# Kernel tuning notes

Hardware: AMD Instinct MI355X
Metric: run time of the kernel (lower is better)

## Reference

```python
import jax, jax.numpy as jnp
import numpy as np

N, E, G = 50000, 800000, 64   # nodes, edges, graphs
IN, HID, H = 128, 64, 4       # in_channels, hidden_channels, heads


def setup_inputs() -> dict:
    key = jax.random.key(0)
    ks = jax.random.split(key, 32)
    r = lambda i, shape, sc=0.05: jax.random.normal(ks[i], shape, jnp.float32) * sc
    inp = {
        "x": jax.random.normal(ks[0], (N, IN), jnp.float32),
        "edge_index": jax.random.randint(ks[1], (2, E), 0, N),
        "batch": jnp.sort(jax.random.randint(ks[2], (N,), 0, G)),
        # GATConv 1: in -> hidden, heads=4, concat
        "W1": r(3, (IN, H * HID)), "a_src1": r(4, (H, HID)), "a_dst1": r(5, (H, HID)), "b1": r(6, (H * HID,)),
        "bn1_g": 1.0 + r(7, (H * HID,)), "bn1_b": r(8, (H * HID,)), "bn1_m": r(9, (H * HID,)),
        "bn1_v": jax.random.uniform(ks[10], (H * HID,), jnp.float32, 0.5, 1.5),
        # GATConv 2: hidden*heads -> hidden, heads=4, concat
        "W2": r(11, (H * HID, H * HID)), "a_src2": r(12, (H, HID)), "a_dst2": r(13, (H, HID)), "b2": r(14, (H * HID,)),
        "bn2_g": 1.0 + r(15, (H * HID,)), "bn2_b": r(16, (H * HID,)), "bn2_m": r(17, (H * HID,)),
        "bn2_v": jax.random.uniform(ks[18], (H * HID,), jnp.float32, 0.5, 1.5),
        # GATConv 3: hidden*heads -> hidden, heads=1
        "W3": r(19, (H * HID, HID)), "a_src3": r(20, (1, HID)), "a_dst3": r(21, (1, HID)), "b3": r(22, (HID,)),
        # projection MLP: Linear(2*hidden, hidden) -> ReLU -> Linear(hidden, hidden)
        "P1": r(23, (2 * HID, HID)), "pb1": r(24, (HID,)),
        "P2": r(25, (HID, HID)), "pb2": r(26, (HID,)),
    }
    return inp


def _gat_conv(x, src, dst, n, W, a_s, a_d, b, concat):
    """PyG-style GATConv (eval mode). src/dst already include self-loops."""
    Hh, C = a_s.shape
    h = (x @ W).reshape(n, Hh, C)                       # [N, H, C]
    al_s = jnp.einsum('nhc,hc->nh', h, a_s)             # [N, H]
    al_d = jnp.einsum('nhc,hc->nh', h, a_d)             # [N, H]
    e = jax.nn.leaky_relu(al_s[src] + al_d[dst], 0.2)   # [E', H]
    # segment softmax over incoming edges of each dst node
    m = jax.ops.segment_max(e, dst, num_segments=n)     # [N, H] (finite: self-loops)
    ex = jnp.exp(e - m[dst])
    den = jax.ops.segment_sum(ex, dst, num_segments=n)
    alpha = ex / den[dst]                               # [E', H]
    out = jax.ops.segment_sum(h[src] * alpha[..., None], dst, num_segments=n)  # [N, H, C]
    out = out.reshape(n, Hh * C) if concat else out.mean(axis=1)
    return out + b


def _bn(x, g, b, m, v):
    return (x - m) * jax.lax.rsqrt(v + 1e-5) * g + b


def _forward(x, edge_index, batch,
             W1, a_src1, a_dst1, b1, bn1_g, bn1_b, bn1_m, bn1_v,
             W2, a_src2, a_dst2, b2, bn2_g, bn2_b, bn2_m, bn2_v,
             W3, a_src3, a_dst3, b3, P1, pb1, P2, pb2):
    n = x.shape[0]
    loop = jnp.arange(n)
    src = jnp.concatenate([edge_index[0], loop])        # add_self_loops=True
    dst = jnp.concatenate([edge_index[1], loop])
    h = _gat_conv(x, src, dst, n, W1, a_src1, a_dst1, b1, True)
    h = jax.nn.elu(_bn(h, bn1_g, bn1_b, bn1_m, bn1_v))  # dropout inactive in eval
    h = _gat_conv(h, src, dst, n, W2, a_src2, a_dst2, b2, True)
    h = jax.nn.elu(_bn(h, bn2_g, bn2_b, bn2_m, bn2_v))
    h = _gat_conv(h, src, dst, n, W3, a_src3, a_dst3, b3, False)  # heads=1
    x_max = jax.ops.segment_max(h, batch, num_segments=G)
    cnt = jax.ops.segment_sum(jnp.ones((n, 1), h.dtype), batch, num_segments=G)
    x_mean = jax.ops.segment_sum(h, batch, num_segments=G) / jnp.maximum(cnt, 1.0)
    z = jnp.concatenate([x_max, x_mean], axis=1)        # [G, 2*HID]
    z = jax.nn.relu(z @ P1 + pb1)
    return z @ P2 + pb2                                  # [G, HID]


def reference(x, edge_index, batch,
              W1, a_src1, a_dst1, b1, bn1_g, bn1_b, bn1_m, bn1_v,
              W2, a_src2, a_dst2, b2, bn2_g, bn2_b, bn2_m, bn2_v,
              W3, a_src3, a_dst3, b3, P1, pb1, P2, pb2):
    return _forward(x, edge_index, batch,
                    W1, a_src1, a_dst1, b1, bn1_g, bn1_b, bn1_m, bn1_v,
                    W2, a_src2, a_dst2, b2, bn2_g, bn2_b, bn2_m, bn2_v,
                    W3, a_src3, a_dst3, b3, P1, pb1, P2, pb2)
```

## Files before the change

### kernel.cpp

```cpp
#include <hip/hip_runtime.h>

typedef unsigned int uint;
typedef unsigned short ushort;

#define NFIX 50000
#define EFIX 800000
#define GFIX 64
#define BCAP 64
#define DCAP 128
#define WSTRIDE 136
#define PSL 16

__device__ __forceinline__ float bflo(uint u) { return __uint_as_float(u << 16); }
__device__ __forceinline__ float bfhi(uint u) { return __uint_as_float(u & 0xffff0000u); }
__device__ __forceinline__ float bf1(ushort u) { return __uint_as_float(((uint)u) << 16); }
__device__ __forceinline__ ushort f2bf(float f) {
    uint u = __float_as_uint(f);
    u += 0x7fffu + ((u >> 16) & 1u);
    return (ushort)(u >> 16);
}
__device__ __forceinline__ float lrelu(float x) { return fmaxf(x, 0.2f * x); }

typedef __attribute__((ext_vector_type(8))) short bf16x8;
typedef __attribute__((ext_vector_type(4))) float f32x4;
union U16B { uint4 u; bf16x8 v; };

__device__ __forceinline__ int ld_idx(const int* __restrict__ p, long i, int w64) {
    return w64 ? p[2 * i] : p[i];
}

__device__ __forceinline__ int frag_off(int k, int c, int K) {
    return ((c >> 4) * (K >> 5) + (k >> 5)) * 512 + ((c & 15) + 16 * ((k >> 3) & 3)) * 8 + (k & 7);
}

#define WJ1 (128 * 256)
#define WJ2 (256 * 256)
#define WJ3 (256 * 64)
#define SCJOBS (EFIX + WJ2 + WJ3)

__global__ void pre_w1_detect(const int* __restrict__ ei, int* __restrict__ flag,
                              const float* __restrict__ W1, ushort* __restrict__ Wf1) {
    if (blockIdx.x == gridDim.x - 1) {
        const int lane = threadIdx.x & 63;
        if (threadIdx.x < 64) {
            int v = (lane < 16) ? ei[2 * lane + 1] : 0;
            unsigned long long any = __ballot(v != 0);
            if (lane == 0) *flag = (any == 0ULL) ? 1 : 0;
        }
        return;
    }
    int j = blockIdx.x * 256 + threadIdx.x;
    int k = j >> 8, c = j & 255;
    Wf1[frag_off(k, c, 128)] = f2bf(W1[j]);
}

__global__ __launch_bounds__(256) void gemm1_build(
    const float* __restrict__ x, const ushort* __restrict__ Wf,
    const float* __restrict__ as_, const float* __restrict__ ad_,
    ushort* __restrict__ Hout, float* __restrict__ als, float* __restrict__ ald,
    int M, int gemmBlocks,
    const int* __restrict__ ei, const int* __restrict__ flag,
    int* __restrict__ cnt, ushort* __restrict__ ssb,
    const float* __restrict__ W2, ushort* __restrict__ Wf2,
    const float* __restrict__ W3, ushort* __restrict__ Wf3) {
    constexpr int K = 128;
    constexpr int NI = 4;
    constexpr int LOG2K = 7;
    __shared__ ushort sa[64][K + 8];

    if (blockIdx.x >= gemmBlocks) {
        int i = (blockIdx.x - gemmBlocks) * 256 + threadIdx.x;
        if (i < EFIX) {
            const int w64 = *flag;
            int d = ld_idx(ei, (long)EFIX + i, w64);
            int s = ld_idx(ei, i, w64);
            int slot = atomicAdd(&cnt[d], 1);
            if (slot < BCAP) ssb[d * BCAP + slot] = (ushort)s;
        } else {
            int j = i - EFIX;
            if (j < WJ2) {
                int k = j >> 8, c = j & 255;
                Wf2[frag_off(k, c, 256)] = f2bf(W2[j]);
            } else if ((j -= WJ2) < WJ3) {
                int k = j >> 6, c = j & 63;
                Wf3[frag_off(k, c, 256)] = f2bf(W3[j]);
            }
        }
        return;
    }

    const int tid = threadIdx.x;
    const int wave = tid >> 6;
    const int lane = tid & 63;
    const int rowBase = blockIdx.x * 64;
    const int colBase = wave * (NI * 16);
    const int tr = lane & 15;
    const int kq = (lane >> 4) * 8;

#pragma unroll
    for (int it = 0; it < (64 * K) / 1024; ++it) {
        int linear = it * 1024 + tid * 4;
        int row = rowBase + (linear >> LOG2K);
        int col = linear & (K - 1);
        row = row < M ? row : M - 1;
        float4 v = *(const float4*)(x + (size_t)row * K + col);
        ushort4 o; o.x = f2bf(v.x); o.y = f2bf(v.y); o.z = f2bf(v.z); o.w = f2bf(v.w);
        *(ushort4*)(&sa[linear >> LOG2K][col]) = o;
    }
    __syncthreads();

    f32x4 acc[4][NI];
#pragma unroll
    for (int i = 0; i < 4; ++i)
#pragma unroll
        for (int j = 0; j < NI; ++j) acc[i][j] = (f32x4){0.f, 0.f, 0.f, 0.f};

    const ushort* bp[NI];
#pragma unroll
    for (int ni = 0; ni < NI; ++ni)
        bp[ni] = Wf + ((size_t)(colBase / 16 + ni) * (K / 32)) * 512 + lane * 8;

    for (int k0 = 0; k0 < K; k0 += 32) {
        bf16x8 a[4], b[NI];
#pragma unroll
        for (int mi = 0; mi < 4; ++mi) { U16B t; t.u = *(const uint4*)(&sa[mi * 16 + tr][k0 + kq]); a[mi] = t.v; }
#pragma unroll
        for (int ni = 0; ni < NI; ++ni) { U16B t; t.u = *(const uint4*)(bp[ni] + (k0 >> 5) * 512); b[ni] = t.v; }
#pragma unroll
        for (int mi = 0; mi < 4; ++mi)
#pragma unroll
            for (int ni = 0; ni < NI; ++ni)
                acc[mi][ni] = __builtin_amdgcn_mfma_f32_16x16x32_bf16(a[mi], b[ni], acc[mi][ni], 0, 0, 0);
    }

    const int orow = (lane >> 4) * 4;
    const int ocol = colBase + tr;
#pragma unroll
    for (int mi = 0; mi < 4; ++mi) {
#pragma unroll
        for (int r = 0; r < 4; ++r) {
            int row = rowBase + mi * 16 + orow + r;
            if (row < M) {
#pragma unroll
                for (int ni = 0; ni < NI; ++ni)
                    Hout[(size_t)row * 256 + ocol + ni * 16] = f2bf(acc[mi][ni][r]);
            }
        }
    }

    float asv[NI], adv[NI];
#pragma unroll
    for (int ni = 0; ni < NI; ++ni) {
        asv[ni] = as_[colBase + ni * 16 + tr];
        adv[ni] = ad_[colBase + ni * 16 + tr];
    }
#pragma unroll
    for (int mi = 0; mi < 4; ++mi) {
#pragma unroll
        for (int r = 0; r < 4; ++r) {
            float ps = 0.f, pd = 0.f;
#pragma unroll
            for (int ni = 0; ni < NI; ++ni) {
                ps += acc[mi][ni][r] * asv[ni];
                pd += acc[mi][ni][r] * adv[ni];
            }
#pragma unroll
            for (int off = 1; off < 16; off <<= 1) {
                ps += __shfl_xor(ps, off, 64);
                pd += __shfl_xor(pd, off, 64);
            }
            int row = rowBase + mi * 16 + orow + r;
            if (tr == 0 && row < M) {
                als[(size_t)row * 4 + wave] = ps;
                ald[(size_t)row * 4 + wave] = pd;
            }
        }
    }
}

template <int K, int NI, int HAL>
__global__ __launch_bounds__(256) void gemm_frag(const ushort* __restrict__ X,
                                                 const ushort* __restrict__ Wf,
                                                 const float* __restrict__ as_,
                                                 const float* __restrict__ ad_,
                                                 ushort* __restrict__ Hout,
                                                 float* __restrict__ als,
                                                 float* __restrict__ ald, int M) {
    constexpr int NC = NI * 16 * 4;
    constexpr int LOG2K = (K == 256) ? 8 : 7;
    __shared__ ushort sa[64][K + 8];
    __shared__ float s_ps[4][64];
    __shared__ float s_pd[4][64];

    const int tid = threadIdx.x;
    const int wave = tid >> 6;
    const int lane = tid & 63;
    const int rowBase = blockIdx.x * 64;
    const int colBase = wave * (NI * 16);
    const int tr = lane & 15;
    const int kq = (lane >> 4) * 8;

    const ushort* src = X + (size_t)rowBase * K;
#pragma unroll
    for (int it = 0; it < (64 * K) / 2048; ++it) {
        int linear = it * 2048 + tid * 8;
        int row = linear >> LOG2K;
        int col = linear & (K - 1);
        *(uint4*)(&sa[row][col]) = *(const uint4*)(src + linear);
    }
    __syncthreads();

    f32x4 acc[4][NI];
#pragma unroll
    for (int i = 0; i < 4; ++i)
#pragma unroll
        for (int j = 0; j < NI; ++j) acc[i][j] = (f32x4){0.f, 0.f, 0.f, 0.f};

    const ushort* bp[NI];
#pragma unroll
    for (int ni = 0; ni < NI; ++ni)
        bp[ni] = Wf + ((size_t)(colBase / 16 + ni) * (K / 32)) * 512 + lane * 8;

    for (int k0 = 0; k0 < K; k0 += 32) {
        bf16x8 a[4], b[NI];
#pragma unroll
        for (int mi = 0; mi < 4; ++mi) { U16B t; t.u = *(const uint4*)(&sa[mi * 16 + tr][k0 + kq]); a[mi] = t.v; }
#pragma unroll
        for (int ni = 0; ni < NI; ++ni) { U16B t; t.u = *(const uint4*)(bp[ni] + (k0 >> 5) * 512); b[ni] = t.v; }
#pragma unroll
        for (int mi = 0; mi < 4; ++mi)
#pragma unroll
            for (int ni = 0; ni < NI; ++ni)
                acc[mi][ni] = __builtin_amdgcn_mfma_f32_16x16x32_bf16(a[mi], b[ni], acc[mi][ni], 0, 0, 0);
    }

    const int orow = (lane >> 4) * 4;
    const int ocol = colBase + tr;
#pragma unroll
    for (int mi = 0; mi < 4; ++mi) {
#pragma unroll
        for (int r = 0; r < 4; ++r) {
            int row = rowBase + mi * 16 + orow + r;
            if (row < M) {
#pragma unroll
                for (int ni = 0; ni < NI; ++ni)
                    Hout[(size_t)row * NC + ocol + ni * 16] = f2bf(acc[mi][ni][r]);
            }
        }
    }

    float asv[NI], adv[NI];
#pragma unroll
    for (int ni = 0; ni < NI; ++ni) {
        asv[ni] = as_[colBase + ni * 16 + tr];
        adv[ni] = ad_[colBase + ni * 16 + tr];
    }
#pragma unroll
    for (int mi = 0; mi < 4; ++mi) {
#pragma unroll
        for (int r = 0; r < 4; ++r) {
            float ps = 0.f, pd = 0.f;
#pragma unroll
            for (int ni = 0; ni < NI; ++ni) {
                ps += acc[mi][ni][r] * asv[ni];
                pd += acc[mi][ni][r] * adv[ni];
            }
#pragma unroll
            for (int off = 1; off < 16; off <<= 1) {
                ps += __shfl_xor(ps, off, 64);
                pd += __shfl_xor(pd, off, 64);
            }
            if constexpr (HAL == 4) {
                int row = rowBase + mi * 16 + orow + r;
                if (tr == 0 && row < M) {
                    als[(size_t)row * 4 + wave] = ps;
                    ald[(size_t)row * 4 + wave] = pd;
                }
            } else {
                if (tr == 0) {
                    s_ps[wave][mi * 16 + orow + r] = ps;
                    s_pd[wave][mi * 16 + orow + r] = pd;
                }
            }
        }
    }
    if constexpr (HAL == 1) {
        __syncthreads();
        if (tid < 64) {
            int row = rowBase + tid;
            if (row < M) {
                als[row] = s_ps[0][tid] + s_ps[1][tid] + s_ps[2][tid] + s_ps[3][tid];
                ald[row] = s_pd[0][tid] + s_pd[1][tid] + s_pd[2][tid] + s_pd[3][tid];
            }
        }
    }
}

template <int H_, int C>
__global__ __launch_bounds__(256) void gat_gather(
    const ushort* __restrict__ hb, const float* __restrict__ als, const float* __restrict__ ald,
    const int* __restrict__ cnt, const ushort* __restrict__ ssb,
    const float* __restrict__ bias, const float* __restrict__ bng, const float* __restrict__ bnb,
    const float* __restrict__ bnm, const float* __restrict__ bnv,
    ushort* __restrict__ xnext, int n) {
    constexpr int TC = H_ * C;
    constexpr int CPL = TC / 64;
    constexpr int GW = 64 / H_;
    constexpr int KMAX = DCAP / GW;
    constexpr int SHIFT = 8;
    __shared__ float s_w[4][H_ * WSTRIDE];
    __shared__ int s_idx[4][DCAP];
    const int wv = threadIdx.x >> 6;
    const int node = blockIdx.x * 4 + wv;
    if (node >= n) return;
    const int lane = threadIdx.x & 63;
    const int head = lane / GW;
    const int hl = lane & (GW - 1);
    const int c0 = lane * CPL;

    const float aldn = ald[(size_t)node * H_ + head];
    const float selfle = lrelu(als[(size_t)node * H_ + head] + aldn);
    const int e0 = node * BCAP;
    int d = cnt[node];
    d = d < BCAP ? d : BCAP;

    float acc[CPL];

    {
        float le_reg[KMAX];
        int s_reg[KMAX];
        float m = selfle;
#pragma unroll
        for (int k = 0; k < KMAX; ++k) {
            int j = hl + k * GW;
            if (j < d) {
                int s = ssb[e0 + j];
                s_reg[k] = s;
                float le = lrelu(als[(size_t)s * H_ + head] + aldn);
                le_reg[k] = le;
                m = fmaxf(m, le);
            }
        }
#pragma unroll
        for (int off = 1; off < GW; off <<= 1) m = fmaxf(m, __shfl_xor(m, off, 64));

        float dsum = (hl == 0) ? __expf(selfle - m) : 0.f;
#pragma unroll
        for (int k = 0; k < KMAX; ++k) {
            int j = hl + k * GW;
            if (j < d) {
                float p = __expf(le_reg[k] - m);
                dsum += p;
                s_w[wv][head * WSTRIDE + j] = p;
                if (head == 0) s_idx[wv][j] = s_reg[k] << SHIFT;
            }
        }
#pragma unroll
        for (int off = 1; off < GW; off <<= 1) dsum += __shfl_xor(dsum, off, 64);
        const float inv = 1.0f / dsum;

        {
            float psf = __expf(selfle - m);
            uint2 hu = *(const uint2*)(hb + (size_t)node * TC + c0);
            acc[0] = psf * bflo(hu.x); acc[1] = psf * bfhi(hu.x);
            acc[2] = psf * bflo(hu.y); acc[3] = psf * bfhi(hu.y);
        }
        const float* wbase = &s_w[wv][head * WSTRIDE];
        const int* ibase = &s_idx[wv][0];
        const ushort* hc = hb + c0;
        int j = 0;
        for (; j + 8 <= d; j += 8) {
            float4 wa = *(const float4*)(wbase + j);
            float4 wb2 = *(const float4*)(wbase + j + 4);
            int4 ia = *(const int4*)(ibase + j);
            int4 ib = *(const int4*)(ibase + j + 4);
            uint2 h0 = *(const uint2*)(hc + ia.x);
            uint2 h1 = *(const uint2*)(hc + ia.y);
            uint2 h2 = *(const uint2*)(hc + ia.z);
            uint2 h3 = *(const uint2*)(hc + ia.w);
            uint2 h4 = *(const uint2*)(hc + ib.x);
            uint2 h5 = *(const uint2*)(hc + ib.y);
            uint2 h6 = *(const uint2*)(hc + ib.z);
            uint2 h7 = *(const uint2*)(hc + ib.w);
            acc[0] = fmaf(wa.x, bflo(h0.x), acc[0]); acc[1] = fmaf(wa.x, bfhi(h0.x), acc[1]);
            acc[2] = fmaf(wa.x, bflo(h0.y), acc[2]); acc[3] = fmaf(wa.x, bfhi(h0.y), acc[3]);
            acc[0] = fmaf(wa.y, bflo(h1.x), acc[0]); acc[1] = fmaf(wa.y, bfhi(h1.x), acc[1]);
            acc[2] = fmaf(wa.y, bflo(h1.y), acc[2]); acc[3] = fmaf(wa.y, bfhi(h1.y), acc[3]);
            acc[0] = fmaf(wa.z, bflo(h2.x), acc[0]); acc[1] = fmaf(wa.z, bfhi(h2.x), acc[1]);
            acc[2] = fmaf(wa.z, bflo(h2.y), acc[2]); acc[3] = fmaf(wa.z, bfhi(h2.y), acc[3]);
            acc[0] = fmaf(wa.w, bflo(h3.x), acc[0]); acc[1] = fmaf(wa.w, bfhi(h3.x), acc[1]);
            acc[2] = fmaf(wa.w, bflo(h3.y), acc[2]); acc[3] = fmaf(wa.w, bfhi(h3.y), acc[3]);
            acc[0] = fmaf(wb2.x, bflo(h4.x), acc[0]); acc[1] = fmaf(wb2.x, bfhi(h4.x), acc[1]);
            acc[2] = fmaf(wb2.x, bflo(h4.y), acc[2]); acc[3] = fmaf(wb2.x, bfhi(h4.y), acc[3]);
            acc[0] = fmaf(wb2.y, bflo(h5.x), acc[0]); acc[1] = fmaf(wb2.y, bfhi(h5.x), acc[1]);
            acc[2] = fmaf(wb2.y, bflo(h5.y), acc[2]); acc[3] = fmaf(wb2.y, bfhi(h5.y), acc[3]);
            acc[0] = fmaf(wb2.z, bflo(h6.x), acc[0]); acc[1] = fmaf(wb2.z, bfhi(h6.x), acc[1]);
            acc[2] = fmaf(wb2.z, bflo(h6.y), acc[2]); acc[3] = fmaf(wb2.z, bfhi(h6.y), acc[3]);
            acc[0] = fmaf(wb2.w, bflo(h7.x), acc[0]); acc[1] = fmaf(wb2.w, bfhi(h7.x), acc[1]);
            acc[2] = fmaf(wb2.w, bflo(h7.y), acc[2]); acc[3] = fmaf(wb2.w, bfhi(h7.y), acc[3]);
        }
        for (; j + 4 <= d; j += 4) {
            float4 wa = *(const float4*)(wbase + j);
            int4 ia = *(const int4*)(ibase + j);
            uint2 h0 = *(const uint2*)(hc + ia.x);
            uint2 h1 = *(const uint2*)(hc + ia.y);
            uint2 h2 = *(const uint2*)(hc + ia.z);
            uint2 h3 = *(const uint2*)(hc + ia.w);
            acc[0] = fmaf(wa.x, bflo(h0.x), acc[0]); acc[1] = fmaf(wa.x, bfhi(h0.x), acc[1]);
            acc[2] = fmaf(wa.x, bflo(h0.y), acc[2]); acc[3] = fmaf(wa.x, bfhi(h0.y), acc[3]);
            acc[0] = fmaf(wa.y, bflo(h1.x), acc[0]); acc[1] = fmaf(wa.y, bfhi(h1.x), acc[1]);
            acc[2] = fmaf(wa.y, bflo(h1.y), acc[2]); acc[3] = fmaf(wa.y, bfhi(h1.y), acc[3]);
            acc[0] = fmaf(wa.z, bflo(h2.x), acc[0]); acc[1] = fmaf(wa.z, bfhi(h2.x), acc[1]);
            acc[2] = fmaf(wa.z, bflo(h2.y), acc[2]); acc[3] = fmaf(wa.z, bfhi(h2.y), acc[3]);
            acc[0] = fmaf(wa.w, bflo(h3.x), acc[0]); acc[1] = fmaf(wa.w, bfhi(h3.x), acc[1]);
            acc[2] = fmaf(wa.w, bflo(h3.y), acc[2]); acc[3] = fmaf(wa.w, bfhi(h3.y), acc[3]);
        }
        for (; j < d; ++j) {
            float w = wbase[j];
            int io = ibase[j];
            uint2 hu = *(const uint2*)(hc + io);
            acc[0] = fmaf(w, bflo(hu.x), acc[0]); acc[1] = fmaf(w, bfhi(hu.x), acc[1]);
            acc[2] = fmaf(w, bflo(hu.y), acc[2]); acc[3] = fmaf(w, bfhi(hu.y), acc[3]);
        }
#pragma unroll
        for (int q = 0; q < CPL; ++q) acc[q] *= inv;
    }

    float4 bi = *(const float4*)(bias + c0);
    float4 gg = *(const float4*)(bng + c0);
    float4 bb = *(const float4*)(bnb + c0);
    float4 mm = *(const float4*)(bnm + c0);
    float4 vv = *(const float4*)(bnv + c0);
    float biA[4] = { bi.x, bi.y, bi.z, bi.w };
    float ggA[4] = { gg.x, gg.y, gg.z, gg.w };
    float bbA[4] = { bb.x, bb.y, bb.z, bb.w };
    float mmA[4] = { mm.x, mm.y, mm.z, mm.w };
    float vvA[4] = { vv.x, vv.y, vv.z, vv.w };
    float r[4];
#pragma unroll
    for (int j2 = 0; j2 < 4; ++j2) {
        float v = acc[j2] + biA[j2];
        v = (v - mmA[j2]) * rsqrtf(vvA[j2] + 1e-5f) * ggA[j2] + bbA[j2];
        v = v > 0.f ? v : (__expf(v) - 1.0f);
        r[j2] = v;
    }
    uint p0 = (uint)f2bf(r[0]) | ((uint)f2bf(r[1]) << 16);
    uint p1 = (uint)f2bf(r[2]) | ((uint)f2bf(r[3]) << 16);
    uint2 o; o.x = p0; o.y = p1;
    *(uint2*)(xnext + (size_t)node * TC + c0) = o;
}

__global__ __launch_bounds__(256) void gat_gather_fin(
    const ushort* __restrict__ hb, const float* __restrict__ als, const float* __restrict__ ald,
    const int* __restrict__ cnt, const ushort* __restrict__ ssb,
    const float* __restrict__ bias, float* __restrict__ yout, int n) {
    __shared__ float s_w[4][BCAP + 16];
    __shared__ int s_idx[4][BCAP + 16];
    const int wv = threadIdx.x >> 6;
    const int node = blockIdx.x * 4 + wv;
    if (node >= n) return;
    const int lane = threadIdx.x & 63;
    const int es = lane >> 4;
    const int cq = (lane & 15) * 4;

    const float aldn = ald[node];
    const float selfle = lrelu(als[node] + aldn);
    const int e0 = node * BCAP;
    int d = cnt[node];
    d = d < BCAP ? d : BCAP;
    const int dpad = (d + 15) & ~15;

    float le = -3.0e38f;
    int sreg = 0;
    if (lane < d) {
        sreg = ssb[e0 + lane];
        le = lrelu(als[sreg] + aldn);
    }
    float m = fmaxf(le, selfle);
#pragma unroll
    for (int off = 1; off < 64; off <<= 1) m = fmaxf(m, __shfl_xor(m, off, 64));

    float p = 0.f;
    if (lane < d) {
        p = __expf(le - m);
        s_w[wv][lane] = p;
        s_idx[wv][lane] = sreg << 6;
    } else if (lane < dpad) {
        s_w[wv][lane] = 0.f;
        s_idx[wv][lane] = 0;
    }
    const float psf = __expf(selfle - m);
    float dsum = p + (lane == 0 ? psf : 0.f);
#pragma unroll
    for (int off = 1; off < 64; off <<= 1) dsum += __shfl_xor(dsum, off, 64);
    const float inv = 1.0f / dsum;

    const ushort* hp = hb + cq;
    const float* wbase = &s_w[wv][0];
    const int* ibase = &s_idx[wv][0];
    float a0 = 0.f, a1 = 0.f, a2 = 0.f, a3 = 0.f;
    for (int j = 0; j < d; j += 16) {
        int i0 = ibase[j + es];
        int i1 = ibase[j + 4 + es];
        int i2 = ibase[j + 8 + es];
        int i3 = ibase[j + 12 + es];
        uint2 h0 = *(const uint2*)(hp + i0);
        uint2 h1 = *(const uint2*)(hp + i1);
        uint2 h2 = *(const uint2*)(hp + i2);
        uint2 h3 = *(const uint2*)(hp + i3);
        float w0 = wbase[j + es];
        float w1 = wbase[j + 4 + es];
        float w2 = wbase[j + 8 + es];
        float w3 = wbase[j + 12 + es];
        a0 = fmaf(w0, bflo(h0.x), a0); a1 = fmaf(w0, bfhi(h0.x), a1);
        a2 = fmaf(w0, bflo(h0.y), a2); a3 = fmaf(w0, bfhi(h0.y), a3);
        a0 = fmaf(w1, bflo(h1.x), a0); a1 = fmaf(w1, bfhi(h1.x), a1);
        a2 = fmaf(w1, bflo(h1.y), a2); a3 = fmaf(w1, bfhi(h1.y), a3);
        a0 = fmaf(w2, bflo(h2.x), a0); a1 = fmaf(w2, bfhi(h2.x), a1);
        a2 = fmaf(w2, bflo(h2.y), a2); a3 = fmaf(w2, bfhi(h2.y), a3);
        a0 = fmaf(w3, bflo(h3.x), a0); a1 = fmaf(w3, bfhi(h3.x), a1);
        a2 = fmaf(w3, bflo(h3.y), a2); a3 = fmaf(w3, bfhi(h3.y), a3);
    }
#pragma unroll
    for (int off = 16; off < 64; off <<= 1) {
        a0 += __shfl_xor(a0, off, 64);
        a1 += __shfl_xor(a1, off, 64);
        a2 += __shfl_xor(a2, off, 64);
        a3 += __shfl_xor(a3, off, 64);
    }
    {
        uint2 hs = *(const uint2*)(hp + node * 64);
        a0 = (a0 + psf * bflo(hs.x)) * inv;
        a1 = (a1 + psf * bfhi(hs.x)) * inv;
        a2 = (a2 + psf * bflo(hs.y)) * inv;
        a3 = (a3 + psf * bfhi(hs.y)) * inv;
    }
    if (es == 0) {
        float4 o = { a0 + bias[cq + 0], a1 + bias[cq + 1],
                     a2 + bias[cq + 2], a3 + bias[cq + 3] };
        *(float4*)(yout + (size_t)node * 64 + cq) = o;
    }
}

__device__ __forceinline__ int lbound_w(const int* a, int n, int v, int w64) {
    int lo = 0, hi = n;
    while (lo < hi) {
        int mid = (lo + hi) >> 1;
        int bv = w64 ? a[2 * mid] : a[mid];
        if (bv < v) lo = mid + 1; else hi = mid;
    }
    return lo;
}

__global__ __launch_bounds__(256) void pool_part(const float* __restrict__ y, const int* __restrict__ batch,
                                                 const int* __restrict__ flag,
                                                 float* __restrict__ part) {
    const int w64 = *flag;
    const int g = blockIdx.x;
    const int sl = blockIdx.y;
    const int t = threadIdx.x;
    const int start = lbound_w(batch, NFIX, g, w64);
    const int end = lbound_w(batch, NFIX, g + 1, w64);
    const int len = end - start;
    const int s0 = start + (int)((long)len * sl / PSL);
    const int s1 = start + (int)((long)len * (sl + 1) / PSL);
    const int ch = t & 63, sub = t >> 6;
    float mx = -3.0e38f, sm = 0.f;
    for (int i = s0 + sub; i < s1; i += 4) {
        float v = y[(size_t)i * 64 + ch];
        mx = fmaxf(mx, v); sm += v;
    }
    __shared__ float smx[256], ssm[256];
    smx[t] = mx; ssm[t] = sm;
    __syncthreads();
    if (t < 64) {
        mx = fmaxf(fmaxf(smx[t], smx[t + 64]), fmaxf(smx[t + 128], smx[t + 192]));
        sm = ssm[t] + ssm[t + 64] + ssm[t + 128] + ssm[t + 192];
        float* pb = part + ((size_t)g * PSL + sl) * 128;
        pb[t] = mx;
        pb[64 + t] = sm;
    }
}

__global__ __launch_bounds__(64) void pool_fin_mlp(const float* __restrict__ part,
                                                   const int* __restrict__ batch,
                                                   const int* __restrict__ flag,
                                                   const float* __restrict__ P1, const float* __restrict__ pb1,
                                                   const float* __restrict__ P2, const float* __restrict__ pb2,
                                                   float* __restrict__ out) {
    const int w64 = *flag;
    const int g = blockIdx.x;
    const int t = threadIdx.x;
    const int start = lbound_w(batch, NFIX, g, w64);
    const int end = lbound_w(batch, NFIX, g + 1, w64);
    const int cnt = end - start;
    __shared__ float pl[128];
    __shared__ float z[64];
    float mx = -3.0e38f, sm = 0.f;
    const float* pb = part + (size_t)g * PSL * 128;
#pragma unroll
    for (int s = 0; s < PSL; ++s) {
        mx = fmaxf(mx, pb[s * 128 + t]);
        sm += pb[s * 128 + 64 + t];
    }
    float mean = cnt > 0 ? sm / (float)cnt : 0.f;
    if (cnt == 0) mx = 0.f;
    pl[t] = mx;
    pl[64 + t] = mean;
    __syncthreads();
    float a = pb1[t];
    for (int k = 0; k < 128; ++k) a = fmaf(pl[k], P1[k * 64 + t], a);
    z[t] = fmaxf(a, 0.f);
    __syncthreads();
    float o = pb2[t];
    for (int k = 0; k < 64; ++k) o = fmaf(z[k], P2[k * 64 + t], o);
    out[(size_t)g * 64 + t] = o;
}

__global__ void write_code(float* out, float code) {
    if (threadIdx.x == 0 && blockIdx.x == 0) out[0] = code;
}

extern "C" void kernel_launch(void* const* d_in, const int* in_sizes, int n_in,
                              void* d_out, int out_size, void* d_ws, size_t ws_size,
                              hipStream_t stream) {
    const float* x = (const float*)d_in[0];
    const int* ei = (const int*)d_in[1];
    const int* batch = (const int*)d_in[2];
    const float* W1 = (const float*)d_in[3];
    const float* as1 = (const float*)d_in[4];
    const float* ad1 = (const float*)d_in[5];
    const float* b1 = (const float*)d_in[6];
    const float* bn1g = (const float*)d_in[7];
    const float* bn1b = (const float*)d_in[8];
    const float* bn1m = (const float*)d_in[9];
    const float* bn1v = (const float*)d_in[10];
    const float* W2 = (const float*)d_in[11];
    const float* as2 = (const float*)d_in[12];
    const float* ad2 = (const float*)d_in[13];
    const float* b2 = (const float*)d_in[14];
    const float* bn2g = (const float*)d_in[15];
    const float* bn2b = (const float*)d_in[16];
    const float* bn2m = (const float*)d_in[17];
    const float* bn2v = (const float*)d_in[18];
    const float* W3 = (const float*)d_in[19];
    const float* as3 = (const float*)d_in[20];
    const float* ad3 = (const float*)d_in[21];
    const float* b3 = (const float*)d_in[22];
    const float* P1 = (const float*)d_in[23];
    const float* pb1 = (const float*)d_in[24];
    const float* P2 = (const float*)d_in[25];
    const float* pb2 = (const float*)d_in[26];
    float* out = (float*)d_out;
    (void)n_in; (void)out_size; (void)in_sizes;

    const int N_ = NFIX;

    char* ws = (char*)d_ws;
    size_t off = 0;
    auto alloc = [&](size_t bytes) -> void* {
        void* p = ws + off;
        off = (off + bytes + 255) & ~(size_t)255;
        return p;
    };
    ushort* hbuf = (ushort*)alloc((size_t)N_ * 256 * 2);
    ushort* xbuf = (ushort*)alloc((size_t)N_ * 256 * 2);
    float* als = (float*)alloc((size_t)N_ * 4 * 4);
    float* ald = (float*)alloc((size_t)N_ * 4 * 4);
    int* cnt = (int*)alloc((size_t)N_ * 4);
    ushort* ssb = (ushort*)alloc((size_t)N_ * BCAP * 2);
    ushort* Wf1 = (ushort*)alloc(128 * 256 * 2);
    ushort* Wf2 = (ushort*)alloc(256 * 256 * 2);
    ushort* Wf3 = (ushort*)alloc(256 * 64 * 2);
    float* part = (float*)alloc((size_t)GFIX * PSL * 128 * 4);
    int* flag = (int*)alloc(256);
    float* y3 = (float*)xbuf;
    const size_t needed = off;

    if (ws_size < needed) {
        write_code<<<1, 64, 0, stream>>>(out, 1000.0f + (float)(needed >> 20));
        return;
    }

    const int ng4 = (N_ + 3) / 4;
    const int rb64 = (N_ + 63) / 64;
    const int scg = (SCJOBS + 255) / 256;
    const int wg1 = WJ1 / 256 + 1;

    hipMemsetAsync(cnt, 0, (size_t)N_ * 4, stream);
    pre_w1_detect<<<wg1, 256, 0, stream>>>(ei, flag, W1, Wf1);

    gemm1_build<<<rb64 + scg, 256, 0, stream>>>(x, Wf1, as1, ad1, hbuf, als, ald,
                                                N_, rb64, ei, flag, cnt, ssb,
                                                W2, Wf2, W3, Wf3);
    gat_gather<4, 64><<<ng4, 256, 0, stream>>>(hbuf, als, ald, cnt, ssb,
                                               b1, bn1g, bn1b, bn1m, bn1v, xbuf, N_);
    gemm_frag<256, 4, 4><<<rb64, 256, 0, stream>>>(xbuf, Wf2, as2, ad2, hbuf, als, ald, N_);
    gat_gather<4, 64><<<ng4, 256, 0, stream>>>(hbuf, als, ald, cnt, ssb,
                                               b2, bn2g, bn2b, bn2m, bn2v, xbuf, N_);
    gemm_frag<256, 1, 1><<<rb64, 256, 0, stream>>>(xbuf, Wf3, as3, ad3, hbuf, als, ald, N_);
    gat_gather_fin<<<ng4, 256, 0, stream>>>(hbuf, als, ald, cnt, ssb, b3, y3, N_);

    pool_part<<<dim3(GFIX, PSL), 256, 0, stream>>>(y3, batch, flag, part);
    pool_fin_mlp<<<GFIX, 64, 0, stream>>>(part, batch, flag, P1, pb1, P2, pb2, out);
}
```

Baseline: 383.0 us.

## Fuse GAT attention gather with the following layer's GEMM per 16-node tile

Merges the gather/softmax/BN/ELU kernel with the next layer's MFMA GEMM. Each block aggregates 16 nodes into shared memory and immediately multiplies them by the next weight matrix, also producing the attention logits. This removes the round trip of the intermediate activation buffer through global memory and two kernel launches. In exchange, each block loads the full weight fragments for only 16 rows, which raises weight traffic, and it uses separate ping-pong buffers for the attention logits.

```diff
diff --git a/kernel.cpp b/kernel.cpp
--- a/kernel.cpp
+++ b/kernel.cpp
@@ -178,176 +178,62 @@
     }
 }
 
-template <int K, int NI, int HAL>
-__global__ __launch_bounds__(256) void gemm_frag(const ushort* __restrict__ X,
-                                                 const ushort* __restrict__ Wf,
-                                                 const float* __restrict__ as_,
-                                                 const float* __restrict__ ad_,
-                                                 ushort* __restrict__ Hout,
-                                                 float* __restrict__ als,
-                                                 float* __restrict__ ald, int M) {
-    constexpr int NC = NI * 16 * 4;
-    constexpr int LOG2K = (K == 256) ? 8 : 7;
-    __shared__ ushort sa[64][K + 8];
-    __shared__ float s_ps[4][64];
-    __shared__ float s_pd[4][64];
-
-    const int tid = threadIdx.x;
-    const int wave = tid >> 6;
-    const int lane = tid & 63;
-    const int rowBase = blockIdx.x * 64;
-    const int colBase = wave * (NI * 16);
-    const int tr = lane & 15;
-    const int kq = (lane >> 4) * 8;
-
-    const ushort* src = X + (size_t)rowBase * K;
-#pragma unroll
-    for (int it = 0; it < (64 * K) / 2048; ++it) {
-        int linear = it * 2048 + tid * 8;
-        int row = linear >> LOG2K;
-        int col = linear & (K - 1);
-        *(uint4*)(&sa[row][col]) = *(const uint4*)(src + linear);
-    }
-    __syncthreads();
-
-    f32x4 acc[4][NI];
-#pragma unroll
-    for (int i = 0; i < 4; ++i)
-#pragma unroll
-        for (int j = 0; j < NI; ++j) acc[i][j] = (f32x4){0.f, 0.f, 0.f, 0.f};
-
-    const ushort* bp[NI];
-#pragma unroll
-    for (int ni = 0; ni < NI; ++ni)
-        bp[ni] = Wf + ((size_t)(colBase / 16 + ni) * (K / 32)) * 512 + lane * 8;
-
-    for (int k0 = 0; k0 < K; k0 += 32) {
-        bf16x8 a[4], b[NI];
-#pragma unroll
-        for (int mi = 0; mi < 4; ++mi) { U16B t; t.u = *(const uint4*)(&sa[mi * 16 + tr][k0 + kq]); a[mi] = t.v; }
-#pragma unroll
-        for (int ni = 0; ni < NI; ++ni) { U16B t; t.u = *(const uint4*)(bp[ni] + (k0 >> 5) * 512); b[ni] = t.v; }
-#pragma unroll
-        for (int mi = 0; mi < 4; ++mi)
-#pragma unroll
-            for (int ni = 0; ni < NI; ++ni)
-                acc[mi][ni] = __builtin_amdgcn_mfma_f32_16x16x32_bf16(a[mi], b[ni], acc[mi][ni], 0, 0, 0);
-    }
-
-    const int orow = (lane >> 4) * 4;
-    const int ocol = colBase + tr;
-#pragma unroll
-    for (int mi = 0; mi < 4; ++mi) {
-#pragma unroll
-        for (int r = 0; r < 4; ++r) {
-            int row = rowBase + mi * 16 + orow + r;
-            if (row < M) {
-#pragma unroll
-                for (int ni = 0; ni < NI; ++ni)
-                    Hout[(size_t)row * NC + ocol + ni * 16] = f2bf(acc[mi][ni][r]);
-            }
-        }
-    }
-
-    float asv[NI], adv[NI];
-#pragma unroll
-    for (int ni = 0; ni < NI; ++ni) {
-        asv[ni] = as_[colBase + ni * 16 + tr];
-        adv[ni] = ad_[colBase + ni * 16 + tr];
-    }
-#pragma unroll
-    for (int mi = 0; mi < 4; ++mi) {
-#pragma unroll
-        for (int r = 0; r < 4; ++r) {
-            float ps = 0.f, pd = 0.f;
-#pragma unroll
-            for (int ni = 0; ni < NI; ++ni) {
-                ps += acc[mi][ni][r] * asv[ni];
-                pd += acc[mi][ni][r] * adv[ni];
-            }
-#pragma unroll
-            for (int off = 1; off < 16; off <<= 1) {
-                ps += __shfl_xor(ps, off, 64);
-                pd += __shfl_xor(pd, off, 64);
-            }
-            if constexpr (HAL == 4) {
-                int row = rowBase + mi * 16 + orow + r;
-                if (tr == 0 && row < M) {
-                    als[(size_t)row * 4 + wave] = ps;
-                    ald[(size_t)row * 4 + wave] = pd;
-                }
-            } else {
-                if (tr == 0) {
-                    s_ps[wave][mi * 16 + orow + r] = ps;
-                    s_pd[wave][mi * 16 + orow + r] = pd;
-                }
-            }
-        }
-    }
-    if constexpr (HAL == 1) {
-        __syncthreads();
-        if (tid < 64) {
-            int row = rowBase + tid;
-            if (row < M) {
-                als[row] = s_ps[0][tid] + s_ps[1][tid] + s_ps[2][tid] + s_ps[3][tid];
-                ald[row] = s_pd[0][tid] + s_pd[1][tid] + s_pd[2][tid] + s_pd[3][tid];
-            }
-        }
-    }
-}
-
-template <int H_, int C>
-__global__ __launch_bounds__(256) void gat_gather(
+template <int NOUT>
+__global__ __launch_bounds__(256) void fused_gather_gemm(
     const ushort* __restrict__ hb, const float* __restrict__ als, const float* __restrict__ ald,
     const int* __restrict__ cnt, const ushort* __restrict__ ssb,
     const float* __restrict__ bias, const float* __restrict__ bng, const float* __restrict__ bnb,
     const float* __restrict__ bnm, const float* __restrict__ bnv,
-    ushort* __restrict__ xnext, int n) {
-    constexpr int TC = H_ * C;
-    constexpr int CPL = TC / 64;
-    constexpr int GW = 64 / H_;
-    constexpr int KMAX = DCAP / GW;
+    const ushort* __restrict__ Wf, const float* __restrict__ as_, const float* __restrict__ ad_,
+    ushort* __restrict__ Hout, float* __restrict__ als_o, float* __restrict__ ald_o, int n) {
+    constexpr int K = 256;
+    constexpr int NI = NOUT / 64;
     constexpr int SHIFT = 8;
-    __shared__ float s_w[4][H_ * WSTRIDE];
+    __shared__ ushort sa[16][K + 8];
+    __shared__ float s_w[4][4 * WSTRIDE];
     __shared__ int s_idx[4][DCAP];
-    const int wv = threadIdx.x >> 6;
-    const int node = blockIdx.x * 4 + wv;
-    if (node >= n) return;
-    const int lane = threadIdx.x & 63;
-    const int head = lane / GW;
-    const int hl = lane & (GW - 1);
-    const int c0 = lane * CPL;
-
-    const float aldn = ald[(size_t)node * H_ + head];
-    const float selfle = lrelu(als[(size_t)node * H_ + head] + aldn);
-    const int e0 = node * BCAP;
-    int d = cnt[node];
-    d = d < BCAP ? d : BCAP;
-
-    float acc[CPL];
-
-    {
-        float le_reg[KMAX];
-        int s_reg[KMAX];
+    __shared__ float s_ps[4][16];
+    __shared__ float s_pd[4][16];
+
+    const int tid = threadIdx.x;
+    const int wv = tid >> 6;
+    const int lane = tid & 63;
+    const int rowBase = blockIdx.x * 16;
+    const int head = lane >> 4;
+    const int hl = lane & 15;
+    const int c0 = lane * 4;
+
+    for (int sub = 0; sub < 4; ++sub) {
+        const int node = rowBase + wv * 4 + sub;
+        const int nodec = node < n ? node : n - 1;
+
+        const float aldn = ald[(size_t)nodec * 4 + head];
+        const float selfle = lrelu(als[(size_t)nodec * 4 + head] + aldn);
+        const int e0 = nodec * BCAP;
+        int d = cnt[nodec];
+        d = d < BCAP ? d : BCAP;
+
+        float le_reg[8];
+        int s_reg[8];
         float m = selfle;
 #pragma unroll
-        for (int k = 0; k < KMAX; ++k) {
-            int j = hl + k * GW;
+        for (int k = 0; k < 8; ++k) {
+            int j = hl + k * 16;
             if (j < d) {
                 int s = ssb[e0 + j];
                 s_reg[k] = s;
-                float le = lrelu(als[(size_t)s * H_ + head] + aldn);
+                float le = lrelu(als[(size_t)s * 4 + head] + aldn);
                 le_reg[k] = le;
                 m = fmaxf(m, le);
             }
         }
 #pragma unroll
-        for (int off = 1; off < GW; off <<= 1) m = fmaxf(m, __shfl_xor(m, off, 64));
+        for (int off = 1; off < 16; off <<= 1) m = fmaxf(m, __shfl_xor(m, off, 64));
 
         float dsum = (hl == 0) ? __expf(selfle - m) : 0.f;
 #pragma unroll
-        for (int k = 0; k < KMAX; ++k) {
-            int j = hl + k * GW;
+        for (int k = 0; k < 8; ++k) {
+            int j = hl + k * 16;
             if (j < d) {
                 float p = __expf(le_reg[k] - m);
                 dsum += p;
@@ -356,12 +242,13 @@
             }
         }
 #pragma unroll
-        for (int off = 1; off < GW; off <<= 1) dsum += __shfl_xor(dsum, off, 64);
+        for (int off = 1; off < 16; off <<= 1) dsum += __shfl_xor(dsum, off, 64);
         const float inv = 1.0f / dsum;
 
+        float acc[4];
         {
             float psf = __expf(selfle - m);
-            uint2 hu = *(const uint2*)(hb + (size_t)node * TC + c0);
+            uint2 hu = *(const uint2*)(hb + (size_t)nodec * 256 + c0);
             acc[0] = psf * bflo(hu.x); acc[1] = psf * bfhi(hu.x);
             acc[2] = psf * bflo(hu.y); acc[3] = psf * bfhi(hu.y);
         }
@@ -423,31 +310,110 @@
             acc[2] = fmaf(w, bflo(hu.y), acc[2]); acc[3] = fmaf(w, bfhi(hu.y), acc[3]);
         }
 #pragma unroll
-        for (int q = 0; q < CPL; ++q) acc[q] *= inv;
-    }
-
-    float4 bi = *(const float4*)(bias + c0);
-    float4 gg = *(const float4*)(bng + c0);
-    float4 bb = *(const float4*)(bnb + c0);
-    float4 mm = *(const float4*)(bnm + c0);
-    float4 vv = *(const float4*)(bnv + c0);
-    float biA[4] = { bi.x, bi.y, bi.z, bi.w };
-    float ggA[4] = { gg.x, gg.y, gg.z, gg.w };
-    float bbA[4] = { bb.x, bb.y, bb.z, bb.w };
-    float mmA[4] = { mm.x, mm.y, mm.z, mm.w };
-    float vvA[4] = { vv.x, vv.y, vv.z, vv.w };
-    float r[4];
-#pragma unroll
-    for (int j2 = 0; j2 < 4; ++j2) {
-        float v = acc[j2] + biA[j2];
-        v = (v - mmA[j2]) * rsqrtf(vvA[j2] + 1e-5f) * ggA[j2] + bbA[j2];
-        v = v > 0.f ? v : (__expf(v) - 1.0f);
-        r[j2] = v;
-    }
-    uint p0 = (uint)f2bf(r[0]) | ((uint)f2bf(r[1]) << 16);
-    uint p1 = (uint)f2bf(r[2]) | ((uint)f2bf(r[3]) << 16);
-    uint2 o; o.x = p0; o.y = p1;
-    *(uint2*)(xnext + (size_t)node * TC + c0) = o;
+        for (int q = 0; q < 4; ++q) acc[q] *= inv;
+
+        float4 bi = *(const float4*)(bias + c0);
+        float4 gg = *(const float4*)(bng + c0);
+        float4 bb = *(const float4*)(bnb + c0);
+        float4 mm = *(const float4*)(bnm + c0);
+        float4 vv = *(const float4*)(bnv + c0);
+        float biA[4] = { bi.x, bi.y, bi.z, bi.w };
+        float ggA[4] = { gg.x, gg.y, gg.z, gg.w };
+        float bbA[4] = { bb.x, bb.y, bb.z, bb.w };
+        float mmA[4] = { mm.x, mm.y, mm.z, mm.w };
+        float vvA[4] = { vv.x, vv.y, vv.z, vv.w };
+        float r[4];
+#pragma unroll
+        for (int q = 0; q < 4; ++q) {
+            float v = acc[q] + biA[q];
+            v = (v - mmA[q]) * rsqrtf(vvA[q] + 1e-5f) * ggA[q] + bbA[q];
+            v = v > 0.f ? v : (__expf(v) - 1.0f);
+            r[q] = v;
+        }
+        uint2 o;
+        o.x = (uint)f2bf(r[0]) | ((uint)f2bf(r[1]) << 16);
+        o.y = (uint)f2bf(r[2]) | ((uint)f2bf(r[3]) << 16);
+        *(uint2*)(&sa[wv * 4 + sub][c0]) = o;
+    }
+    __syncthreads();
+
+    const int tr = lane & 15;
+    const int kq = (lane >> 4) * 8;
+    const int colBase = wv * (NI * 16);
+
+    f32x4 acc[NI];
+#pragma unroll
+    for (int ni = 0; ni < NI; ++ni) acc[ni] = (f32x4){0.f, 0.f, 0.f, 0.f};
+
+    const ushort* bp[NI];
+#pragma unroll
+    for (int ni = 0; ni < NI; ++ni)
+        bp[ni] = Wf + ((size_t)(colBase / 16 + ni) * (K / 32)) * 512 + lane * 8;
+
+    for (int k0 = 0; k0 < K; k0 += 32) {
+        bf16x8 a, b[NI];
+        { U16B t; t.u = *(const uint4*)(&sa[tr][k0 + kq]); a = t.v; }
+#pragma unroll
+        for (int ni = 0; ni < NI; ++ni) { U16B t; t.u = *(const uint4*)(bp[ni] + (k0 >> 5) * 512); b[ni] = t.v; }
+#pragma unroll
+        for (int ni = 0; ni < NI; ++ni)
+            acc[ni] = __builtin_amdgcn_mfma_f32_16x16x32_bf16(a, b[ni], acc[ni], 0, 0, 0);
+    }
+
+    const int orow = (lane >> 4) * 4;
+    const int ocol = colBase + tr;
+#pragma unroll
+    for (int r = 0; r < 4; ++r) {
+        int row = rowBase + orow + r;
+        if (row < n) {
+#pragma unroll
+            for (int ni = 0; ni < NI; ++ni)
+                Hout[(size_t)row * NOUT + ocol + ni * 16] = f2bf(acc[ni][r]);
+        }
+    }
+
+    float asv[NI], adv[NI];
+#pragma unroll
+    for (int ni = 0; ni < NI; ++ni) {
+        asv[ni] = as_[colBase + ni * 16 + tr];
+        adv[ni] = ad_[colBase + ni * 16 + tr];
+    }
+#pragma unroll
+    for (int r = 0; r < 4; ++r) {
+        float ps = 0.f, pd = 0.f;
+#pragma unroll
+        for (int ni = 0; ni < NI; ++ni) {
+            ps += acc[ni][r] * asv[ni];
+            pd += acc[ni][r] * adv[ni];
+        }
+#pragma unroll
+        for (int off = 1; off < 16; off <<= 1) {
+            ps += __shfl_xor(ps, off, 64);
+            pd += __shfl_xor(pd, off, 64);
+        }
+        if constexpr (NOUT == 256) {
+            int row = rowBase + orow + r;
+            if (tr == 0 && row < n) {
+                als_o[(size_t)row * 4 + wv] = ps;
+                ald_o[(size_t)row * 4 + wv] = pd;
+            }
+        } else {
+            if (tr == 0) {
+                s_ps[wv][orow + r] = ps;
+                s_pd[wv][orow + r] = pd;
+            }
+        }
+    }
+    if constexpr (NOUT == 64) {
+        __syncthreads();
+        if (tid < 16) {
+            int row = rowBase + tid;
+            if (row < n) {
+                als_o[row] = s_ps[0][tid] + s_ps[1][tid] + s_ps[2][tid] + s_ps[3][tid];
+                ald_o[row] = s_pd[0][tid] + s_pd[1][tid] + s_pd[2][tid] + s_pd[3][tid];
+            }
+        }
+    }
 }
 
 __global__ __launch_bounds__(256) void gat_gather_fin(
@@ -663,10 +629,12 @@
         off = (off + bytes + 255) & ~(size_t)255;
         return p;
     };
-    ushort* hbuf = (ushort*)alloc((size_t)N_ * 256 * 2);
-    ushort* xbuf = (ushort*)alloc((size_t)N_ * 256 * 2);
-    float* als = (float*)alloc((size_t)N_ * 4 * 4);
-    float* ald = (float*)alloc((size_t)N_ * 4 * 4);
+    ushort* bufA = (ushort*)alloc((size_t)N_ * 256 * 2);
+    ushort* bufB = (ushort*)alloc((size_t)N_ * 256 * 2);
+    float* als1 = (float*)alloc((size_t)N_ * 4 * 4);
+    float* ald1 = (float*)alloc((size_t)N_ * 4 * 4);
+    float* als2 = (float*)alloc((size_t)N_ * 4 * 4);
+    float* ald2 = (float*)alloc((size_t)N_ * 4 * 4);
     int* cnt = (int*)alloc((size_t)N_ * 4);
     ushort* ssb = (ushort*)alloc((size_t)N_ * BCAP * 2);
     ushort* Wf1 = (ushort*)alloc(128 * 256 * 2);
@@ -674,7 +642,7 @@
     ushort* Wf3 = (ushort*)alloc(256 * 64 * 2);
     float* part = (float*)alloc((size_t)GFIX * PSL * 128 * 4);
     int* flag = (int*)alloc(256);
-    float* y3 = (float*)xbuf;
+    float* y3 = (float*)bufB;
     const size_t needed = off;
 
     if (ws_size < needed) {
@@ -683,6 +651,7 @@
     }
 
     const int ng4 = (N_ + 3) / 4;
+    const int ngg = (N_ + 15) / 16;
     const int rb64 = (N_ + 63) / 64;
     const int scg = (SCJOBS + 255) / 256;
     const int wg1 = WJ1 / 256 + 1;
@@ -690,16 +659,16 @@
     hipMemsetAsync(cnt, 0, (size_t)N_ * 4, stream);
     pre_w1_detect<<<wg1, 256, 0, stream>>>(ei, flag, W1, Wf1);
 
-    gemm1_build<<<rb64 + scg, 256, 0, stream>>>(x, Wf1, as1, ad1, hbuf, als, ald,
+    gemm1_build<<<rb64 + scg, 256, 0, stream>>>(x, Wf1, as1, ad1, bufA, als1, ald1,
                                                 N_, rb64, ei, flag, cnt, ssb,
                                                 W2, Wf2, W3, Wf3);
-    gat_gather<4, 64><<<ng4, 256, 0, stream>>>(hbuf, als, ald, cnt, ssb,
-                                               b1, bn1g, bn1b, bn1m, bn1v, xbuf, N_);
-    gemm_frag<256, 4, 4><<<rb64, 256, 0, stream>>>(xbuf, Wf2, as2, ad2, hbuf, als, ald, N_);
-    gat_gather<4, 64><<<ng4, 256, 0, stream>>>(hbuf, als, ald, cnt, ssb,
-                                               b2, bn2g, bn2b, bn2m, bn2v, xbuf, N_);
-    gemm_frag<256, 1, 1><<<rb64, 256, 0, stream>>>(xbuf, Wf3, as3, ad3, hbuf, als, ald, N_);
-    gat_gather_fin<<<ng4, 256, 0, stream>>>(hbuf, als, ald, cnt, ssb, b3, y3, N_);
+    fused_gather_gemm<256><<<ngg, 256, 0, stream>>>(bufA, als1, ald1, cnt, ssb,
+                                                    b1, bn1g, bn1b, bn1m, bn1v,
+                                                    Wf2, as2, ad2, bufB, als2, ald2, N_);
+    fused_gather_gemm<64><<<ngg, 256, 0, stream>>>(bufB, als2, ald2, cnt, ssb,
+                                                   b2, bn2g, bn2b, bn2m, bn2v,
+                                                   Wf3, as3, ad3, bufA, als1, ald1, N_);
+    gat_gather_fin<<<ng4, 256, 0, stream>>>(bufA, als1, ald1, cnt, ssb, b3, y3, N_);
 
     pool_part<<<dim3(GFIX, PSL), 256, 0, stream>>>(y3, batch, flag, part);
     pool_fin_mlp<<<GFIX, 64, 0, stream>>>(part, batch, flag, P1, pb1, P2, pb2, out);
```

New measurement: 410.2 us. 7.1% more time.
